# Kernel optimization log

Hardware: AMD Instinct MI355X
Metric: run time of the kernel (lower is better)

The kernel has to match this reference:

```python
import jax, jax.numpy as jnp
import numpy as np

HIDDEN = 3584
N_HEADS = 16
N_KV = 8
HEAD_DIM = 256
INTER = 14336
EPS = 1e-6
SCALING = 256.0 ** -0.5  # query_pre_attn_scalar ** -0.5
SOFTCAP = 50.0
WINDOW = 1024
B, S = 2, 2048


def rmsnorm(x, w, eps=EPS):
    # Gemma2 style: scale by (1 + weight), weight zero-initialized
    var = jnp.mean(x * x, axis=-1, keepdims=True)
    return x * jax.lax.rsqrt(var + eps) * (1.0 + w)


def rotate_half(x):
    half = x.shape[-1] // 2
    return jnp.concatenate([-x[..., half:], x[..., :half]], axis=-1)


def setup_inputs() -> dict:
    key = jax.random.key(0)
    ks = jax.random.split(key, 12)
    hidden_states = jax.random.normal(ks[0], (B, S, HIDDEN), jnp.float32)
    # RoPE tables (theta = 10000)
    inv_freq = 1.0 / (10000.0 ** (np.arange(0, HEAD_DIM, 2, dtype=np.float32) / HEAD_DIM))
    t = np.arange(S, dtype=np.float32)
    freqs = np.outer(t, inv_freq)  # [S, HEAD_DIM/2]
    emb = np.concatenate([freqs, freqs], axis=-1)  # [S, HEAD_DIM]
    cos = jnp.asarray(np.cos(emb))
    sin = jnp.asarray(np.sin(emb))
    sd = lambda fan_in: 1.0 / np.sqrt(fan_in)
    Wq = jax.random.normal(ks[1], (N_HEADS * HEAD_DIM, HIDDEN), jnp.float32) * sd(HIDDEN)
    Wk = jax.random.normal(ks[2], (N_KV * HEAD_DIM, HIDDEN), jnp.float32) * sd(HIDDEN)
    Wv = jax.random.normal(ks[3], (N_KV * HEAD_DIM, HIDDEN), jnp.float32) * sd(HIDDEN)
    Wo = jax.random.normal(ks[4], (HIDDEN, N_HEADS * HEAD_DIM), jnp.float32) * sd(N_HEADS * HEAD_DIM)
    Wgate = jax.random.normal(ks[5], (INTER, HIDDEN), jnp.float32) * sd(HIDDEN)
    Wup = jax.random.normal(ks[6], (INTER, HIDDEN), jnp.float32) * sd(HIDDEN)
    Wdown = jax.random.normal(ks[7], (HIDDEN, INTER), jnp.float32) * sd(INTER)
    # RMSNorm weights zero-init per Gemma2 (effective scale 1.0), small perturbation
    w_in_ln = jax.random.normal(ks[8], (HIDDEN,), jnp.float32) * 0.02
    w_post_attn_ln = jax.random.normal(ks[9], (HIDDEN,), jnp.float32) * 0.02
    w_pre_ff_ln = jax.random.normal(ks[10], (HIDDEN,), jnp.float32) * 0.02
    w_post_ff_ln = jax.random.normal(ks[11], (HIDDEN,), jnp.float32) * 0.02
    return dict(hidden_states=hidden_states, cos=cos, sin=sin, Wq=Wq, Wk=Wk, Wv=Wv,
                Wo=Wo, Wgate=Wgate, Wup=Wup, Wdown=Wdown, w_in_ln=w_in_ln,
                w_post_attn_ln=w_post_attn_ln, w_pre_ff_ln=w_pre_ff_ln,
                w_post_ff_ln=w_post_ff_ln)


def _decoder_layer(hidden_states, cos, sin, Wq, Wk, Wv, Wo, Wgate, Wup, Wdown,
                   w_in_ln, w_post_attn_ln, w_pre_ff_ln, w_post_ff_ln):
    b, s, _ = hidden_states.shape
    residual = hidden_states
    x = rmsnorm(hidden_states, w_in_ln)

    # QKV projections (bias=False), bsnd layout
    q = jnp.einsum('bsh,oh->bso', x, Wq).reshape(b, s, N_HEADS, HEAD_DIM)
    k = jnp.einsum('bsh,oh->bso', x, Wk).reshape(b, s, N_KV, HEAD_DIM)
    v = jnp.einsum('bsh,oh->bso', x, Wv).reshape(b, s, N_KV, HEAD_DIM)

    # RoPE with explicit cos/sin, half-rotation; broadcast over batch & heads
    c = cos[None, :, None, :]
    sn = sin[None, :, None, :]
    q = q * c + rotate_half(q) * sn
    k = k * c + rotate_half(k) * sn

    # GQA: repeat KV heads
    rep = N_HEADS // N_KV
    k = jnp.repeat(k, rep, axis=2)  # [b, s, H, D]
    v = jnp.repeat(v, rep, axis=2)

    # scores with custom scaling + tanh softcap
    scores = jnp.einsum('bqhd,bkhd->bhqk', q, k) * SCALING
    scores = SOFTCAP * jnp.tanh(scores / SOFTCAP)

    # causal + sliding-window mask: attend to j with i-WINDOW < j <= i
    i = jnp.arange(s)[:, None]
    j = jnp.arange(s)[None, :]
    allowed = (j <= i) & (j > i - WINDOW)
    scores = jnp.where(allowed[None, None], scores, jnp.float32(-1e30))

    probs = jax.nn.softmax(scores, axis=-1)
    attn = jnp.einsum('bhqk,bkhd->bqhd', probs, v).reshape(b, s, N_HEADS * HEAD_DIM)
    attn = jnp.einsum('bso,ho->bsh', attn, Wo)

    hidden_states = residual + rmsnorm(attn, w_post_attn_ln)

    residual = hidden_states
    y = rmsnorm(hidden_states, w_pre_ff_ln)
    gate = jax.nn.gelu(jnp.einsum('bsh,ih->bsi', y, Wgate), approximate=True)
    up = jnp.einsum('bsh,ih->bsi', y, Wup)
    mlp = jnp.einsum('bsi,hi->bsh', gate * up, Wdown)
    hidden_states = residual + rmsnorm(mlp, w_post_ff_ln)
    return hidden_states


def reference(hidden_states, cos, sin, Wq, Wk, Wv, Wo, Wgate, Wup, Wdown,
              w_in_ln, w_post_attn_ln, w_pre_ff_ln, w_post_ff_ln):
    return _decoder_layer(hidden_states, cos, sin, Wq, Wk, Wv, Wo, Wgate, Wup,
                          Wdown, w_in_ln, w_post_attn_ln, w_pre_ff_ln, w_post_ff_ln)
```

## Files before the change

kernel.cpp:

```cpp
#include <hip/hip_runtime.h>
#include <hip/hip_bf16.h>

typedef __hip_bfloat16 bf16;
typedef __bf16 bf16x8_t __attribute__((ext_vector_type(8)));
typedef float f32x4_t __attribute__((ext_vector_type(4)));
typedef unsigned short u16x8_t __attribute__((ext_vector_type(8)));

#define HID 3584
#define SEQ 2048
#define NBATCH 2
#define MTOK 4096
#define NHEADS 16
#define NKVH 8
#define HDIM 256
#define QOUT 4096
#define KOUT 2048
#define INTERD 14336
#define EPSF 1e-6f

static __device__ __forceinline__ unsigned short f2bu(float f) {
  union { bf16 b; unsigned short u; } cv;
  cv.b = __float2bfloat16(f);
  return cv.u;
}

static __device__ __forceinline__ f32x4_t mfma16(bf16x8_t a, bf16x8_t b, f32x4_t c) {
  return __builtin_amdgcn_mfma_f32_16x16x32_bf16(a, b, c, 0, 0, 0);
}

static __device__ __forceinline__ void gl_lds16(const void* g, void* l) {
  __builtin_amdgcn_global_load_lds((__attribute__((address_space(1))) void*)g,
                                   (__attribute__((address_space(3))) void*)l,
                                   16, 0, 0);
}

static __device__ __forceinline__ float block_reduce_sum(float v) {
  __shared__ float buf[4];
  #pragma unroll
  for (int m = 1; m < 64; m <<= 1) v += __shfl_xor(v, m, 64);
  __syncthreads();
  if ((threadIdx.x & 63) == 0) buf[threadIdx.x >> 6] = v;
  __syncthreads();
  return buf[0] + buf[1] + buf[2] + buf[3];
}

__global__ __launch_bounds__(256) void cvt_w(
    const float* __restrict__ src, bf16* __restrict__ dst, int n) {
  const int stride = gridDim.x * 256 * 8;
  for (int i = (blockIdx.x * 256 + threadIdx.x) * 8; i < n; i += stride) {
    const float4 a = *(const float4*)(src + i);
    const float4 b = *(const float4*)(src + i + 4);
    u16x8_t o;
    o[0] = f2bu(a.x); o[1] = f2bu(a.y); o[2] = f2bu(a.z); o[3] = f2bu(a.w);
    o[4] = f2bu(b.x); o[5] = f2bu(b.y); o[6] = f2bu(b.z); o[7] = f2bu(b.w);
    *(u16x8_t*)(dst + i) = o;
  }
}

enum { EPI_BF16 = 0, EPI_F32 = 1, EPI_VT = 2, EPI_GELUMUL = 3 };

template <int EPI>
__global__ __launch_bounds__(512, 2) void gemm8p(
    const bf16* __restrict__ A, const bf16* __restrict__ Bw,
    void* __restrict__ Cout, const bf16* __restrict__ aux,
    int Ndim, int Kdim) {
  __shared__ __align__(16) char L[131072];

  const int NT = Kdim >> 6;
  const int NB = gridDim.x;
  const int bid = blockIdx.x;
  const int sw = (bid & 7) * (NB >> 3) + (bid >> 3);
  const int m0 = (sw & 15) * 256;
  const int n0 = (sw >> 4) * 256;

  const int tid = threadIdx.x;
  const int wid = tid >> 6, l = tid & 63;
  const int wm = wid >> 2, wn = wid & 3;
  const int lr = l & 15, lg = l >> 4;

  const int rlane = wid * 16 + (l >> 3);
  const int lc8 = (((l & 7) ^ (l >> 3)) << 3);
  const bf16* srcA = A + (size_t)(m0 + rlane) * Kdim + lc8;
  const bf16* srcB = Bw + (size_t)(n0 + rlane) * Kdim + lc8;
  const size_t K128 = (size_t)Kdim << 7;
  const size_t K8 = (size_t)Kdim << 3;

  auto STAGE = [&](int op, int rh, int tl) {
    if (tl >= NT) return;
    const bf16* s = (op ? srcB : srcA) + (size_t)rh * K128 + ((size_t)tl << 6);
    char* d = L + ((tl & 1) << 16) + (op << 15) + (rh << 14) + (wid << 11);
    gl_lds16(s, d);
    gl_lds16(s + K8, d + 1024);
  };

  const int arow = wm * 128 + lr;
  const int brow = wn * 64 + lr;
  const int swz = lr & 7;
  const int csw0 = ((0 * 4 + lg) ^ swz) << 4;
  const int csw1 = ((1 * 4 + lg) ^ swz) << 4;
  auto LDA = [&](int mi, int kk, int c) {
    return *(const bf16x8_t*)(L + (c << 16) + arow * 128 + mi * 2048 +
                              (kk ? csw1 : csw0));
  };
  auto LDB = [&](int ni, int kk, int c) {
    return *(const bf16x8_t*)(L + (c << 16) + 32768 + brow * 128 + ni * 2048 +
                              (kk ? csw1 : csw0));
  };

  f32x4_t acc[8][4];
  #pragma unroll
  for (int i = 0; i < 8; i++)
    #pragma unroll
    for (int j = 0; j < 4; j++) acc[i][j] = (f32x4_t){0.f, 0.f, 0.f, 0.f};

  bf16x8_t fa[8][2], fb[4][2];

  STAGE(1, 0, 0); STAGE(1, 1, 0); STAGE(0, 0, 0); STAGE(0, 1, 0);
  STAGE(1, 0, 1); STAGE(1, 1, 1); STAGE(0, 0, 1);

#define MFMA_Q(MB, NBQ)                                                        \
  _Pragma("unroll") for (int mi = 0; mi < 4; ++mi)                             \
  _Pragma("unroll") for (int ni = 0; ni < 2; ++ni) {                           \
    acc[MB + mi][NBQ + ni] =                                                   \
        mfma16(fa[MB + mi][0], fb[NBQ + ni][0], acc[MB + mi][NBQ + ni]);       \
    acc[MB + mi][NBQ + ni] =                                                   \
        mfma16(fa[MB + mi][1], fb[NBQ + ni][1], acc[MB + mi][NBQ + ni]);       \
  }

#define TILE(T, C)                                                             \
  {                                                                            \
    if ((T) + 1 < NT) asm volatile("s_waitcnt vmcnt(6)" ::: "memory");         \
    else asm volatile("s_waitcnt vmcnt(0)" ::: "memory");                      \
    __builtin_amdgcn_s_barrier();    \
    __builtin_amdgcn_sched_barrier(0);                                         \
                          \
    _Pragma("unroll") for (int mi = 0; mi < 4; ++mi) {                         \
      fa[mi][0] = LDA(mi, 0, (C)); fa[mi][1] = LDA(mi, 1, (C));                \
    }                                                                          \
    _Pragma("unroll") for (int ni = 0; ni < 4; ++ni) {                         \
      fb[ni][0] = LDB(ni, 0, (C)); fb[ni][1] = LDB(ni, 1, (C));                \
    }                                                                          \
    STAGE(0, 1, (T) + 1);                                                      \
    __builtin_amdgcn_s_barrier();                                              \
    asm volatile("s_waitcnt lgkmcnt(0)" ::: "memory");                         \
    __builtin_amdgcn_sched_barrier(0);                                         \
    __builtin_amdgcn_s_setprio(1);                                             \
    MFMA_Q(0, 0);                                                              \
    __builtin_amdgcn_s_setprio(0);                                             \
    __builtin_amdgcn_s_barrier();                                              \
                      \
    STAGE(1, 0, (T) + 2);                                                      \
    __builtin_amdgcn_s_barrier();                                              \
    __builtin_amdgcn_s_setprio(1);                                             \
    MFMA_Q(0, 2);                                                              \
    __builtin_amdgcn_s_setprio(0);                                             \
    __builtin_amdgcn_s_barrier();                                              \
                                     \
    _Pragma("unroll") for (int mi = 0; mi < 4; ++mi) {                         \
      fa[4 + mi][0] = LDA(4 + mi, 0, (C)); fa[4 + mi][1] = LDA(4 + mi, 1, (C));\
    }                                                                          \
    STAGE(1, 1, (T) + 2);                                                      \
    __builtin_amdgcn_s_barrier();                                              \
    asm volatile("s_waitcnt lgkmcnt(0)" ::: "memory");                         \
    __builtin_amdgcn_sched_barrier(0);                                         \
    __builtin_amdgcn_s_setprio(1);                                             \
    MFMA_Q(4, 0);                                                              \
    __builtin_amdgcn_s_setprio(0);                                             \
    __builtin_amdgcn_s_barrier();                                              \
                        \
    STAGE(0, 0, (T) + 2);                                                      \
    __builtin_amdgcn_s_barrier();                                              \
    __builtin_amdgcn_s_setprio(1);                                             \
    MFMA_Q(4, 2);                                                              \
    __builtin_amdgcn_s_setprio(0);                                             \
    __builtin_amdgcn_s_barrier();                                              \
  }

  for (int t = 0; t < NT; t += 2) {
    TILE(t, 0);
    TILE(t + 1, 1);
  }
#undef TILE
#undef MFMA_Q

  const int row0 = m0 + wm * 128 + lg * 4;
  const int col0 = n0 + wn * 64 + lr;
  #pragma unroll
  for (int mi = 0; mi < 8; mi++) {
    #pragma unroll
    for (int ni = 0; ni < 4; ni++) {
      #pragma unroll
      for (int r = 0; r < 4; r++) {
        const int row = row0 + mi * 16 + r;
        const int col = col0 + ni * 16;
        const float v = acc[mi][ni][r];
        if constexpr (EPI == EPI_BF16) {
          ((bf16*)Cout)[(size_t)row * Ndim + col] = __float2bfloat16(v);
        } else if constexpr (EPI == EPI_F32) {
          ((float*)Cout)[(size_t)row * Ndim + col] = v;
        } else if constexpr (EPI == EPI_VT) {
          const int kvh = col >> 8, d = col & 255;
          const int bb = row >> 11, s = row & 2047;
          ((bf16*)Cout)[(((size_t)((bb * 8 + kvh) * 256 + d)) << 11) + s] =
              __float2bfloat16(v);
        } else {
          const float g = __bfloat162float(aux[(size_t)row * Ndim + col]);
          const float u = 0.7978845608028654f * (g + 0.044715f * g * g * g);
          const float gl = 0.5f * g * (1.f + tanhf(u));
          ((bf16*)Cout)[(size_t)row * Ndim + col] = __float2bfloat16(gl * v);
        }
      }
    }
  }
  (void)aux;
}

__global__ __launch_bounds__(256) void rmsnorm_in(
    const float* __restrict__ x, const float* __restrict__ w,
    bf16* __restrict__ out) {
  const int row = blockIdx.x, t = threadIdx.x;
  const float4* xr = (const float4*)(x + (size_t)row * HID);
  float4 v[4];
  float ss = 0.f;
  #pragma unroll
  for (int j = 0; j < 4; j++) {
    const int idx = t + 256 * j;
    if (idx < HID / 4) {
      v[j] = xr[idx];
      ss += v[j].x * v[j].x + v[j].y * v[j].y + v[j].z * v[j].z + v[j].w * v[j].w;
    }
  }
  ss = block_reduce_sum(ss);
  const float sc = rsqrtf(ss * (1.f / HID) + EPSF);
  const float4* w4 = (const float4*)w;
  bf16* orow = out + (size_t)row * HID;
  #pragma unroll
  for (int j = 0; j < 4; j++) {
    const int idx = t + 256 * j;
    if (idx < HID / 4) {
      const float4 wv = w4[idx];
      ushort4 o;
      o.x = f2bu(v[j].x * sc * (1.f + wv.x));
      o.y = f2bu(v[j].y * sc * (1.f + wv.y));
      o.z = f2bu(v[j].z * sc * (1.f + wv.z));
      o.w = f2bu(v[j].w * sc * (1.f + wv.w));
      *(ushort4*)(orow + idx * 4) = o;
    }
  }
}

__global__ __launch_bounds__(128) void rope_kernel(
    bf16* __restrict__ q, bf16* __restrict__ k,
    const float* __restrict__ cosb, const float* __restrict__ sinb) {
  const int tok = blockIdx.x;
  const int hs = blockIdx.y;
  const int d = threadIdx.x;
  const int s = tok & (SEQ - 1);
  bf16* ptr = (hs < NHEADS)
                  ? q + (size_t)tok * QOUT + hs * HDIM
                  : k + (size_t)tok * KOUT + (hs - NHEADS) * HDIM;
  const float c = cosb[s * HDIM + d];
  const float sn = sinb[s * HDIM + d];
  const float x0 = __bfloat162float(ptr[d]);
  const float x1 = __bfloat162float(ptr[d + 128]);
  ptr[d] = __float2bfloat16(x0 * c - x1 * sn);
  ptr[d + 128] = __float2bfloat16(x1 * c + x0 * sn);
}

__global__ __launch_bounds__(256) void attn_kernel(
    const bf16* __restrict__ q, const bf16* __restrict__ k,
    const bf16* __restrict__ vt, bf16* __restrict__ out) {
  __shared__ __align__(16) bf16 plds[4][16 * 32];

  const int qt = blockIdx.x, h = blockIdx.y, b = blockIdx.z;
  const int w = threadIdx.x >> 6, l = threadIdx.x & 63;
  const int kvh = h >> 1;
  const int qbase = qt * 64 + w * 16;
  const int lr = l & 15, lg = l >> 4, lk = lg * 8;

  bf16x8_t qf[8];
  const bf16* qrow = q + (size_t)(b * SEQ + qbase + lr) * QOUT + h * HDIM;
  #pragma unroll
  for (int c = 0; c < 8; c++) qf[c] = *(const bf16x8_t*)(qrow + c * 32 + lk);

  f32x4_t acc[16];
  #pragma unroll
  for (int i = 0; i < 16; i++) acc[i] = (f32x4_t){0.f, 0.f, 0.f, 0.f};
  float L[4] = {0.f, 0.f, 0.f, 0.f};

  const bf16* kp = k + (size_t)(b * SEQ) * KOUT + kvh * HDIM;
  const bf16* vp = vt + (size_t)(b * NKVH + kvh) * HDIM * SEQ;
  bf16* pl = &plds[w][0];

  int kstart = qbase - 1023;
  if (kstart < 0) kstart = 0;
  kstart &= ~31;
  const int kend = qbase + 15;

  for (int kb = kstart; kb <= kend; kb += 32) {
    f32x4_t s0 = (f32x4_t){0.f, 0.f, 0.f, 0.f};
    f32x4_t s1 = (f32x4_t){0.f, 0.f, 0.f, 0.f};
    #pragma unroll
    for (int c = 0; c < 8; c++) {
      bf16x8_t k0 = *(const bf16x8_t*)(kp + (size_t)(kb + lr) * KOUT + c * 32 + lk);
      bf16x8_t k1 = *(const bf16x8_t*)(kp + (size_t)(kb + 16 + lr) * KOUT + c * 32 + lk);
      s0 = mfma16(qf[c], k0, s0);
      s1 = mfma16(qf[c], k1, s1);
    }
    float p[8];
    #pragma unroll
    for (int sub = 0; sub < 2; sub++) {
      const int j = kb + sub * 16 + lr;
      #pragma unroll
      for (int r = 0; r < 4; r++) {
        const int i = qbase + lg * 4 + r;
        float sc = (sub ? s1[r] : s0[r]) * 0.0625f;
        sc = 50.f * tanhf(sc * 0.02f);
        const bool ok = (j <= i) && (j > i - 1024);
        p[sub * 4 + r] = ok ? __expf(sc) : 0.f;
      }
    }
    #pragma unroll
    for (int r = 0; r < 4; r++) {
      float ps = p[r] + p[4 + r];
      ps += __shfl_xor(ps, 1, 64);
      ps += __shfl_xor(ps, 2, 64);
      ps += __shfl_xor(ps, 4, 64);
      ps += __shfl_xor(ps, 8, 64);
      L[r] += ps;
    }
    #pragma unroll
    for (int sub = 0; sub < 2; sub++)
      #pragma unroll
      for (int r = 0; r < 4; r++)
        pl[(lg * 4 + r) * 32 + sub * 16 + lr] = __float2bfloat16(p[sub * 4 + r]);
    asm volatile("s_waitcnt lgkmcnt(0)" ::: "memory");
    const bf16x8_t pa = *(const bf16x8_t*)(pl + lr * 32 + lk);
    #pragma unroll
    for (int dt = 0; dt < 16; dt++) {
      bf16x8_t bv = *(const bf16x8_t*)(vp + (size_t)(dt * 16 + lr) * SEQ + kb + lk);
      acc[dt] = mfma16(pa, bv, acc[dt]);
    }
  }

  float rL[4];
  #pragma unroll
  for (int r = 0; r < 4; r++) rL[r] = 1.f / L[r];
  #pragma unroll
  for (int dt = 0; dt < 16; dt++) {
    #pragma unroll
    for (int r = 0; r < 4; r++) {
      const int tok = b * SEQ + qbase + lg * 4 + r;
      out[(size_t)tok * QOUT + h * HDIM + dt * 16 + lr] =
          __float2bfloat16(acc[dt][r] * rL[r]);
    }
  }
}

__global__ __launch_bounds__(256) void fuse_attn(
    const float* __restrict__ hidden, const float* __restrict__ ap,
    const float* __restrict__ w_post, const float* __restrict__ w_pre,
    float* __restrict__ h1, bf16* __restrict__ y) {
  const int row = blockIdx.x, t = threadIdx.x;
  const float4* ar = (const float4*)(ap + (size_t)row * HID);
  const float4* hr = (const float4*)(hidden + (size_t)row * HID);
  float4 a[4];
  float ss = 0.f;
  #pragma unroll
  for (int j = 0; j < 4; j++) {
    const int idx = t + 256 * j;
    if (idx < HID / 4) {
      a[j] = ar[idx];
      ss += a[j].x * a[j].x + a[j].y * a[j].y + a[j].z * a[j].z + a[j].w * a[j].w;
    }
  }
  ss = block_reduce_sum(ss);
  const float sc = rsqrtf(ss * (1.f / HID) + EPSF);
  const float4* wpo = (const float4*)w_post;
  float4* h1r = (float4*)(h1 + (size_t)row * HID);
  float4 hv[4];
  float ss2 = 0.f;
  #pragma unroll
  for (int j = 0; j < 4; j++) {
    const int idx = t + 256 * j;
    if (idx < HID / 4) {
      const float4 wv = wpo[idx];
      const float4 x = hr[idx];
      hv[j].x = x.x + a[j].x * sc * (1.f + wv.x);
      hv[j].y = x.y + a[j].y * sc * (1.f + wv.y);
      hv[j].z = x.z + a[j].z * sc * (1.f + wv.z);
      hv[j].w = x.w + a[j].w * sc * (1.f + wv.w);
      ss2 += hv[j].x * hv[j].x + hv[j].y * hv[j].y + hv[j].z * hv[j].z + hv[j].w * hv[j].w;
      h1r[idx] = hv[j];
    }
  }
  ss2 = block_reduce_sum(ss2);
  const float sc2 = rsqrtf(ss2 * (1.f / HID) + EPSF);
  const float4* wpr = (const float4*)w_pre;
  bf16* yr = y + (size_t)row * HID;
  #pragma unroll
  for (int j = 0; j < 4; j++) {
    const int idx = t + 256 * j;
    if (idx < HID / 4) {
      const float4 wv = wpr[idx];
      ushort4 o;
      o.x = f2bu(hv[j].x * sc2 * (1.f + wv.x));
      o.y = f2bu(hv[j].y * sc2 * (1.f + wv.y));
      o.z = f2bu(hv[j].z * sc2 * (1.f + wv.z));
      o.w = f2bu(hv[j].w * sc2 * (1.f + wv.w));
      *(ushort4*)(yr + idx * 4) = o;
    }
  }
}

__global__ __launch_bounds__(256) void fuse_out(
    const float* __restrict__ h1, const float* __restrict__ mlp,
    const float* __restrict__ w, float* __restrict__ out) {
  const int row = blockIdx.x, t = threadIdx.x;
  const float4* mr = (const float4*)(mlp + (size_t)row * HID);
  float4 m[4];
  float ss = 0.f;
  #pragma unroll
  for (int j = 0; j < 4; j++) {
    const int idx = t + 256 * j;
    if (idx < HID / 4) {
      m[j] = mr[idx];
      ss += m[j].x * m[j].x + m[j].y * m[j].y + m[j].z * m[j].z + m[j].w * m[j].w;
    }
  }
  ss = block_reduce_sum(ss);
  const float sc = rsqrtf(ss * (1.f / HID) + EPSF);
  const float4* hr = (const float4*)(h1 + (size_t)row * HID);
  const float4* w4 = (const float4*)w;
  float4* orow = (float4*)(out + (size_t)row * HID);
  #pragma unroll
  for (int j = 0; j < 4; j++) {
    const int idx = t + 256 * j;
    if (idx < HID / 4) {
      const float4 wv = w4[idx];
      const float4 x = hr[idx];
      float4 o;
      o.x = x.x + m[j].x * sc * (1.f + wv.x);
      o.y = x.y + m[j].y * sc * (1.f + wv.y);
      o.z = x.z + m[j].z * sc * (1.f + wv.z);
      o.w = x.w + m[j].w * sc * (1.f + wv.w);
      orow[idx] = o;
    }
  }
}

extern "C" void kernel_launch(void* const* d_in, const int* in_sizes, int n_in,
                              void* d_out, int out_size, void* d_ws,
                              size_t ws_size, hipStream_t stream) {
  const float* hidden = (const float*)d_in[0];
  const float* cosb = (const float*)d_in[1];
  const float* sinb = (const float*)d_in[2];
  const float* Wq = (const float*)d_in[3];
  const float* Wk = (const float*)d_in[4];
  const float* Wv = (const float*)d_in[5];
  const float* Wo = (const float*)d_in[6];
  const float* Wgate = (const float*)d_in[7];
  const float* Wup = (const float*)d_in[8];
  const float* Wdown = (const float*)d_in[9];
  const float* w_in = (const float*)d_in[10];
  const float* w_post_attn = (const float*)d_in[11];
  const float* w_pre_ff = (const float*)d_in[12];
  const float* w_post_ff = (const float*)d_in[13];
  float* out = (float*)d_out;

  (void)in_sizes; (void)n_in; (void)out_size; (void)ws_size;

  const size_t WB = 102760448;
  char* ws = (char*)d_ws;
  bf16* wbuf = (bf16*)ws;
  char* ab = ws + WB;

  bf16* xn = (bf16*)(ab);
  bf16* q = (bf16*)(ab + 29360128);
  float* attn_proj = (float*)(ab);
  float* mlp = (float*)(ab);
  bf16* kbuf = (bf16*)(ab + 62914560);
  bf16* vt = (bf16*)(ab + 62914560 + 16777216);
  bf16* attn_out = (bf16*)(ab + 62914560 + 33554432);
  float* h1 = (float*)(ab + 62914560);
  bf16* y = (bf16*)(ab + 130023424);
  bf16* gate = (bf16*)(ab + 159383552);

  rmsnorm_in<<<MTOK, 256, 0, stream>>>(hidden, w_in, xn);

  cvt_w<<<4096, 256, 0, stream>>>(Wq, wbuf, QOUT * HID);
  gemm8p<EPI_BF16><<<(QOUT / 256) * 16, 512, 0, stream>>>(
      xn, wbuf, q, nullptr, QOUT, HID);
  cvt_w<<<4096, 256, 0, stream>>>(Wk, wbuf, KOUT * HID);
  gemm8p<EPI_BF16><<<(KOUT / 256) * 16, 512, 0, stream>>>(
      xn, wbuf, kbuf, nullptr, KOUT, HID);
  cvt_w<<<4096, 256, 0, stream>>>(Wv, wbuf, KOUT * HID);
  gemm8p<EPI_VT><<<(KOUT / 256) * 16, 512, 0, stream>>>(
      xn, wbuf, vt, nullptr, KOUT, HID);
  rope_kernel<<<dim3(MTOK, NHEADS + NKVH), 128, 0, stream>>>(q, kbuf, cosb, sinb);
  attn_kernel<<<dim3(SEQ / 64, NHEADS, NBATCH), 256, 0, stream>>>(
      q, kbuf, vt, attn_out);
  cvt_w<<<4096, 256, 0, stream>>>(Wo, wbuf, HID * QOUT);
  gemm8p<EPI_F32><<<(HID / 256) * 16, 512, 0, stream>>>(
      attn_out, wbuf, attn_proj, nullptr, HID, QOUT);
  fuse_attn<<<MTOK, 256, 0, stream>>>(hidden, attn_proj, w_post_attn,
                                      w_pre_ff, h1, y);
  cvt_w<<<4096, 256, 0, stream>>>(Wgate, wbuf, INTERD * HID);
  gemm8p<EPI_BF16><<<(INTERD / 256) * 16, 512, 0, stream>>>(
      y, wbuf, gate, nullptr, INTERD, HID);
  cvt_w<<<4096, 256, 0, stream>>>(Wup, wbuf, INTERD * HID);
  gemm8p<EPI_GELUMUL><<<(INTERD / 256) * 16, 512, 0, stream>>>(
      y, wbuf, gate, gate, INTERD, HID);
  cvt_w<<<4096, 256, 0, stream>>>(Wdown, wbuf, HID * INTERD);
  gemm8p<EPI_F32><<<(HID / 256) * 16, 512, 0, stream>>>(
      gate, wbuf, mlp, nullptr, HID, INTERD);

  fuse_out<<<MTOK, 256, 0, stream>>>(h1, mlp, w_post_ff, out);
}
```

Measured before the change: 2.639 ms.

## Fuse QKV projections into one GEMM and restructure GEMM prefetch pipeline

After: 2.787 ms. +5.6%, slower.

```diff
diff --git a/kernel.cpp b/kernel.cpp
--- a/kernel.cpp
+++ b/kernel.cpp
@@ -57,12 +57,13 @@
   }
 }
 
-enum { EPI_BF16 = 0, EPI_F32 = 1, EPI_VT = 2, EPI_GELUMUL = 3 };
+enum { EPI_BF16 = 0, EPI_F32 = 1, EPI_VT = 2, EPI_GELUMUL = 3, EPI_QKV = 4 };
 
 template <int EPI>
 __global__ __launch_bounds__(512, 2) void gemm8p(
     const bf16* __restrict__ A, const bf16* __restrict__ Bw,
     void* __restrict__ Cout, const bf16* __restrict__ aux,
+    void* __restrict__ C2, void* __restrict__ C3,
     int Ndim, int Kdim) {
   __shared__ __align__(16) char L[131072];
 
@@ -116,7 +117,10 @@
   bf16x8_t fa[8][2], fb[4][2];
 
   STAGE(1, 0, 0); STAGE(1, 1, 0); STAGE(0, 0, 0); STAGE(0, 1, 0);
-  STAGE(1, 0, 1); STAGE(1, 1, 1); STAGE(0, 0, 1);
+  STAGE(1, 0, 1); STAGE(1, 1, 1); STAGE(0, 0, 1); STAGE(0, 1, 1);
+  asm volatile("s_waitcnt vmcnt(8)" ::: "memory");
+  __builtin_amdgcn_s_barrier();
+  __builtin_amdgcn_sched_barrier(0);
 
 #define MFMA_Q(MB, NBQ)                                                        \
   _Pragma("unroll") for (int mi = 0; mi < 4; ++mi)                             \
@@ -129,18 +133,13 @@
 
 #define TILE(T, C)                                                             \
   {                                                                            \
-    if ((T) + 1 < NT) asm volatile("s_waitcnt vmcnt(6)" ::: "memory");         \
-    else asm volatile("s_waitcnt vmcnt(0)" ::: "memory");                      \
-    __builtin_amdgcn_s_barrier();    \
-    __builtin_amdgcn_sched_barrier(0);                                         \
-                          \
+                                \
     _Pragma("unroll") for (int mi = 0; mi < 4; ++mi) {                         \
       fa[mi][0] = LDA(mi, 0, (C)); fa[mi][1] = LDA(mi, 1, (C));                \
     }                                                                          \
-    _Pragma("unroll") for (int ni = 0; ni < 4; ++ni) {                         \
+    _Pragma("unroll") for (int ni = 0; ni < 2; ++ni) {                         \
       fb[ni][0] = LDB(ni, 0, (C)); fb[ni][1] = LDB(ni, 1, (C));                \
     }                                                                          \
-    STAGE(0, 1, (T) + 1);                                                      \
     __builtin_amdgcn_s_barrier();                                              \
     asm volatile("s_waitcnt lgkmcnt(0)" ::: "memory");                         \
     __builtin_amdgcn_sched_barrier(0);                                         \
@@ -148,17 +147,24 @@
     MFMA_Q(0, 0);                                                              \
     __builtin_amdgcn_s_setprio(0);                                             \
     __builtin_amdgcn_s_barrier();                                              \
-                      \
-    STAGE(1, 0, (T) + 2);                                                      \
-    __builtin_amdgcn_s_barrier();                                              \
+    __builtin_amdgcn_sched_barrier(0);                                         \
+                                        \
+    _Pragma("unroll") for (int ni = 2; ni < 4; ++ni) {                         \
+      fb[ni][0] = LDB(ni, 0, (C)); fb[ni][1] = LDB(ni, 1, (C));                \
+    }                                                                          \
+    __builtin_amdgcn_s_barrier();                                              \
+    asm volatile("s_waitcnt lgkmcnt(0)" ::: "memory");                         \
+    __builtin_amdgcn_sched_barrier(0);                                         \
     __builtin_amdgcn_s_setprio(1);                                             \
     MFMA_Q(0, 2);                                                              \
     __builtin_amdgcn_s_setprio(0);                                             \
     __builtin_amdgcn_s_barrier();                                              \
-                                     \
-    _Pragma("unroll") for (int mi = 0; mi < 4; ++mi) {                         \
-      fa[4 + mi][0] = LDA(4 + mi, 0, (C)); fa[4 + mi][1] = LDA(4 + mi, 1, (C));\
+    __builtin_amdgcn_sched_barrier(0);                                         \
+                     \
+    _Pragma("unroll") for (int mi = 4; mi < 8; ++mi) {                         \
+      fa[mi][0] = LDA(mi, 0, (C)); fa[mi][1] = LDA(mi, 1, (C));                \
     }                                                                          \
+    STAGE(1, 0, (T) + 2);                                                      \
     STAGE(1, 1, (T) + 2);                                                      \
     __builtin_amdgcn_s_barrier();                                              \
     asm volatile("s_waitcnt lgkmcnt(0)" ::: "memory");                         \
@@ -167,13 +173,21 @@
     MFMA_Q(4, 0);                                                              \
     __builtin_amdgcn_s_setprio(0);                                             \
     __builtin_amdgcn_s_barrier();                                              \
-                        \
+    __builtin_amdgcn_sched_barrier(0);                                         \
+             \
     STAGE(0, 0, (T) + 2);                                                      \
+    STAGE(0, 1, (T) + 2);                                                      \
     __builtin_amdgcn_s_barrier();                                              \
     __builtin_amdgcn_s_setprio(1);                                             \
     MFMA_Q(4, 2);                                                              \
     __builtin_amdgcn_s_setprio(0);                                             \
-    __builtin_amdgcn_s_barrier();                                              \
+    if ((T) + 2 < NT) {                                                        \
+      asm volatile("s_waitcnt vmcnt(8)" ::: "memory");                         \
+    } else {                                                                   \
+      asm volatile("s_waitcnt vmcnt(0)" ::: "memory");                         \
+    }                                                                          \
+    __builtin_amdgcn_s_barrier();                                              \
+    __builtin_amdgcn_sched_barrier(0);                                         \
   }
 
   for (int t = 0; t < NT; t += 2) {
@@ -203,6 +217,19 @@
           const int bb = row >> 11, s = row & 2047;
           ((bf16*)Cout)[(((size_t)((bb * 8 + kvh) * 256 + d)) << 11) + s] =
               __float2bfloat16(v);
+        } else if constexpr (EPI == EPI_QKV) {
+          if (col < 4096) {
+            ((bf16*)Cout)[(size_t)row * 4096 + col] = __float2bfloat16(v);
+          } else if (col < 6144) {
+            ((bf16*)C2)[(size_t)row * 2048 + (col - 4096)] =
+                __float2bfloat16(v);
+          } else {
+            const int cc = col - 6144;
+            const int kvh = cc >> 8, d = cc & 255;
+            const int bb = row >> 11, s = row & 2047;
+            ((bf16*)C3)[(((size_t)((bb * 8 + kvh) * 256 + d)) << 11) + s] =
+                __float2bfloat16(v);
+          }
         } else {
           const float g = __bfloat162float(aux[(size_t)row * Ndim + col]);
           const float u = 0.7978845608028654f * (g + 0.044715f * g * g * g);
@@ -212,7 +239,7 @@
       }
     }
   }
-  (void)aux;
+  (void)aux; (void)C2; (void)C3;
 }
 
 __global__ __launch_bounds__(256) void rmsnorm_in(
@@ -489,31 +516,28 @@
   rmsnorm_in<<<MTOK, 256, 0, stream>>>(hidden, w_in, xn);
 
   cvt_w<<<4096, 256, 0, stream>>>(Wq, wbuf, QOUT * HID);
-  gemm8p<EPI_BF16><<<(QOUT / 256) * 16, 512, 0, stream>>>(
-      xn, wbuf, q, nullptr, QOUT, HID);
-  cvt_w<<<4096, 256, 0, stream>>>(Wk, wbuf, KOUT * HID);
-  gemm8p<EPI_BF16><<<(KOUT / 256) * 16, 512, 0, stream>>>(
-      xn, wbuf, kbuf, nullptr, KOUT, HID);
-  cvt_w<<<4096, 256, 0, stream>>>(Wv, wbuf, KOUT * HID);
-  gemm8p<EPI_VT><<<(KOUT / 256) * 16, 512, 0, stream>>>(
-      xn, wbuf, vt, nullptr, KOUT, HID);
+  cvt_w<<<2048, 256, 0, stream>>>(Wk, wbuf + (size_t)QOUT * HID, KOUT * HID);
+  cvt_w<<<2048, 256, 0, stream>>>(Wv, wbuf + (size_t)(QOUT + KOUT) * HID,
+                                  KOUT * HID);
+  gemm8p<EPI_QKV><<<(8192 / 256) * 16, 512, 0, stream>>>(
+      xn, wbuf, q, nullptr, kbuf, vt, 8192, HID);
   rope_kernel<<<dim3(MTOK, NHEADS + NKVH), 128, 0, stream>>>(q, kbuf, cosb, sinb);
   attn_kernel<<<dim3(SEQ / 64, NHEADS, NBATCH), 256, 0, stream>>>(
       q, kbuf, vt, attn_out);
   cvt_w<<<4096, 256, 0, stream>>>(Wo, wbuf, HID * QOUT);
   gemm8p<EPI_F32><<<(HID / 256) * 16, 512, 0, stream>>>(
-      attn_out, wbuf, attn_proj, nullptr, HID, QOUT);
+      attn_out, wbuf, attn_proj, nullptr, nullptr, nullptr, HID, QOUT);
   fuse_attn<<<MTOK, 256, 0, stream>>>(hidden, attn_proj, w_post_attn,
                                       w_pre_ff, h1, y);
   cvt_w<<<4096, 256, 0, stream>>>(Wgate, wbuf, INTERD * HID);
   gemm8p<EPI_BF16><<<(INTERD / 256) * 16, 512, 0, stream>>>(
-      y, wbuf, gate, nullptr, INTERD, HID);
+      y, wbuf, gate, nullptr, nullptr, nullptr, INTERD, HID);
   cvt_w<<<4096, 256, 0, stream>>>(Wup, wbuf, INTERD * HID);
   gemm8p<EPI_GELUMUL><<<(INTERD / 256) * 16, 512, 0, stream>>>(
-      y, wbuf, gate, gate, INTERD, HID);
+      y, wbuf, gate, gate, nullptr, nullptr, INTERD, HID);
   cvt_w<<<4096, 256, 0, stream>>>(Wdown, wbuf, HID * INTERD);
   gemm8p<EPI_F32><<<(HID / 256) * 16, 512, 0, stream>>>(
-      gate, wbuf, mlp, nullptr, HID, INTERD);
+      gate, wbuf, mlp, nullptr, nullptr, nullptr, HID, INTERD);
 
   fuse_out<<<MTOK, 256, 0, stream>>>(h1, mlp, w_post_ff, out);
 }
```
